# Kernel optimization log

Hardware: AMD Instinct MI355X
Metric: run time of the kernel (lower is better)

Reference implementation:

```python
import jax, jax.numpy as jnp
import numpy as np

B, S, D = 4, 4096, 512
NUM_RANDOM = 32
SEED = 42
SCALE = 1.0 / float(np.sqrt(D))


def _make_random_mask(seq_len, num_random, seed):
    # Faithful to module semantics: diagonal always attended, plus up to
    # (num_random-1) randomly sampled earlier positions per row.
    rng = np.random.default_rng(seed)
    mask = np.zeros((seq_len, seq_len), dtype=bool)
    mask[np.arange(seq_len), np.arange(seq_len)] = True
    for i in range(1, seq_len):
        n = min(num_random - 1, i)
        cols = rng.choice(i, size=n, replace=False)
        mask[i, cols] = True
    return mask


def setup_inputs() -> dict:
    key = jax.random.key(0)
    kq, kk, kv = jax.random.split(key, 3)
    q = jax.random.normal(kq, (B, S, D), dtype=jnp.float32)
    k = jax.random.normal(kk, (B, S, D), dtype=jnp.float32)
    v = jax.random.normal(kv, (B, S, D), dtype=jnp.float32)
    mask = jnp.asarray(_make_random_mask(S, NUM_RANDOM, SEED))  # [S, S] bool
    return {"q": q, "k": k, "v": v, "mask": mask}


def reference(q, k, v, mask):
    # scores: [B, S, S]
    scores = jnp.einsum("bqd,bkd->bqk", q, k) * SCALE
    scores = jnp.where(mask[None, :, :], scores, -jnp.inf)
    attn = jax.nn.softmax(scores, axis=-1)  # every row has >=1 True (diag)
    out = jnp.einsum("bqk,bkd->bqd", attn, v)
    return out, attn, mask
```

## Files before the change

### kernel.cpp

```cpp
#include <hip/hip_runtime.h>
#include <hip/hip_fp16.h>


#define SDIM 4096
#define DDIM 512
#define BATCH 4
#define CCAP 128
#define NREC 32
#define RECSTRIDE 68

#define DT_BF16 0
#define DT_FP16 1
#define DT_FP32 2

#define OUT_ELEMS ((size_t)BATCH * SDIM * DDIM)

__device__ __forceinline__ float bf2f(unsigned int u) {
    return __uint_as_float((u & 0xFFFFu) << 16);
}
__device__ __forceinline__ float h2f(unsigned int u) {
    __half_raw hr; hr.x = (unsigned short)(u & 0xFFFFu);
    return __half2float(hr);
}
__device__ __forceinline__ float decode16(unsigned int bits, int dt) {
    return (dt == DT_BF16) ? bf2f(bits) : h2f(bits);
}

__device__ __forceinline__ bool elem_nz(const unsigned char* m, int w, int i, int j) {
    const unsigned char* p = m + ((size_t)i * SDIM + (size_t)j) * w;
    unsigned v = p[0];
    if (w >= 2) v |= p[1];
    if (w == 4) { v |= p[2]; v |= p[3]; }
    return v != 0;
}
__device__ void detect_mask(const unsigned char* m, int* w_out, int* inv_out) {
    for (int wi = 0; wi < 3; ++wi) {
        const int W = 1 << wi;
        for (int s = 0; s < 2; ++s) {
            const bool att_nz = (s == 0);
            bool ok = true;
            ok &= (elem_nz(m, W, 0, 0) == att_nz);
            ok &= (elem_nz(m, W, 0, 1) != att_nz);
            ok &= (elem_nz(m, W, 0, 2) != att_nz);
            ok &= (elem_nz(m, W, 0, 3) != att_nz);
            ok &= (elem_nz(m, W, 1, 0) == att_nz);
            ok &= (elem_nz(m, W, 1, 1) == att_nz);
            ok &= (elem_nz(m, W, 1, 2) != att_nz);
            ok &= (elem_nz(m, W, 1, 3) != att_nz);
            if (ok) { *w_out = W; *inv_out = s; return; }
        }
    }
    *w_out = 1; *inv_out = 0;
}

#define QG 68

__device__ __forceinline__ void v_accum(
    const unsigned char* __restrict__ vb, int b, int t, int dt,
    const int* __restrict__ cols, const float* __restrict__ probs, int n,
    float& acc0, float& acc1)
{
    acc0 = 0.f; acc1 = 0.f;
    if (dt == DT_FP32) {
        const float2* vbase = (const float2*)((const float*)vb + (size_t)b * SDIM * DDIM);
        int j = 0;
        for (; j + 8 <= n; j += 8) {
            float2 vv[8]; float pp[8];
            #pragma unroll
            for (int u = 0; u < 8; ++u) {
                vv[u] = vbase[(size_t)cols[j + u] * (DDIM / 2) + t];
                pp[u] = probs[j + u];
            }
            #pragma unroll
            for (int u = 0; u < 8; ++u) {
                acc0 += pp[u] * vv[u].x;
                acc1 += pp[u] * vv[u].y;
            }
        }
        for (; j < n; ++j) {
            float2 vv = vbase[(size_t)cols[j] * (DDIM / 2) + t];
            acc0 += probs[j] * vv.x; acc1 += probs[j] * vv.y;
        }
    } else {
        const unsigned short* vb16 = (const unsigned short*)vb;
        int j = 0;
        for (; j + 8 <= n; j += 8) {
            unsigned int vv[8]; float pp[8];
            #pragma unroll
            for (int u = 0; u < 8; ++u) {
                vv[u] = ((const unsigned int*)(vb16 + ((size_t)b * SDIM + cols[j + u]) * DDIM))[t];
                pp[u] = probs[j + u];
            }
            #pragma unroll
            for (int u = 0; u < 8; ++u) {
                acc0 += pp[u] * decode16(vv[u], dt);
                acc1 += pp[u] * decode16(vv[u] >> 16, dt);
            }
        }
        for (; j < n; ++j) {
            unsigned int vv = ((const unsigned int*)(vb16 + ((size_t)b * SDIM + cols[j]) * DDIM))[t];
            acc0 += probs[j] * decode16(vv, dt);
            acc1 += probs[j] * decode16(vv >> 16, dt);
        }
    }
}

__global__ __launch_bounds__(256, 8) void score_kernel(
    const unsigned char* __restrict__ qb,
    const unsigned char* __restrict__ kb,
    const unsigned char* __restrict__ vb,
    const unsigned char* __restrict__ mask,
    float* __restrict__ out,
    float* __restrict__ rec_base,
    long long rec_stride,
    int write_attn)
{
    const int row = blockIdx.x;
    const int b = row >> 12;
    const int i = row & (SDIM - 1);
    const int t = threadIdx.x;
    const int lane = t & 63;
    const int wv = t >> 6;

    __shared__ float q_lds[8 * QG];
    __shared__ int   cols[CCAP];
    __shared__ float scores[CCAP];
    __shared__ float red[4];
    __shared__ int count;
    __shared__ int s_dt;

    if (t == 0) count = 0;
    if (t < 64) {
        unsigned int w = ((const unsigned int*)qb)[t];
        unsigned int by = (w >> 8) & 0x7Fu;
        int cnt_top = __popcll(__ballot(by == 0x3Eu || by == 0x3Fu));
        int cnt_mid = __popcll(__ballot(by >= 0x34u && by <= 0x43u));
        if (t == 0)
            s_dt = (cnt_top >= 20) ? DT_BF16 : ((cnt_mid >= 25) ? DT_FP16 : DT_FP32);
    }
    int mw, minv;
    detect_mask(mask, &mw, &minv);
    __syncthreads();
    const int dt = s_dt;

    if (dt == DT_FP32) {
        float2 qv = ((const float2*)((const float*)qb + ((size_t)b * SDIM + i) * DDIM))[t];
        const int e = 2 * t, a = (e >> 6) * QG + (e & 63);
        q_lds[a] = qv.x; q_lds[a + 1] = qv.y;
    } else {
        unsigned int qv = ((const unsigned int*)((const unsigned short*)qb
                            + ((size_t)b * SDIM + i) * DDIM))[t];
        const int e = 2 * t, a = (e >> 6) * QG + (e & 63);
        q_lds[a] = decode16(qv, dt); q_lds[a + 1] = decode16(qv >> 16, dt);
    }

    if (mw == 1) {
        const unsigned char* mrow = mask + (size_t)i * SDIM;
        uint4 mv = ((const uint4*)mrow)[t];
        unsigned int wd[4] = {mv.x, mv.y, mv.z, mv.w};
        #pragma unroll
        for (int c = 0; c < 4; ++c)
            #pragma unroll
            for (int bi = 0; bi < 4; ++bi) {
                bool nz = ((wd[c] >> (8 * bi)) & 0xFFu) != 0;
                if (nz != (bool)minv) {
                    int pos = atomicAdd(&count, 1);
                    if (pos < CCAP) cols[pos] = t * 16 + c * 4 + bi;
                }
            }
    } else if (mw == 2) {
        const unsigned short* mrow = (const unsigned short*)mask + (size_t)i * SDIM;
        const uint4* m4 = (const uint4*)mrow + t * 2;
        #pragma unroll
        for (int c = 0; c < 2; ++c) {
            uint4 mv = m4[c];
            unsigned int e[4] = {mv.x, mv.y, mv.z, mv.w};
            #pragma unroll
            for (int bi = 0; bi < 4; ++bi) {
                const int base = t * 16 + c * 8 + bi * 2;
                if (((e[bi] & 0xFFFFu) != 0) != (bool)minv) { int p = atomicAdd(&count, 1); if (p < CCAP) cols[p] = base; }
                if (((e[bi] >> 16) != 0)     != (bool)minv) { int p = atomicAdd(&count, 1); if (p < CCAP) cols[p] = base + 1; }
            }
        }
    } else {
        const unsigned int* mrow = (const unsigned int*)mask + (size_t)i * SDIM;
        const uint4* m4 = (const uint4*)mrow + t * 4;
        #pragma unroll
        for (int c = 0; c < 4; ++c) {
            uint4 mv = m4[c];
            unsigned int e[4] = {mv.x, mv.y, mv.z, mv.w};
            #pragma unroll
            for (int bi = 0; bi < 4; ++bi) {
                if ((e[bi] != 0u) != (bool)minv) {
                    int p = atomicAdd(&count, 1);
                    if (p < CCAP) cols[p] = t * 16 + c * 4 + bi;
                }
            }
        }
    }
    __syncthreads();
    const int n = min(count, CCAP);

    const float SCALE = 0.04419417382415922f;
    const int idx = t >> 3, sub = t & 7;
    for (int base = 0; base < n; base += 32) {
        const int j = base + idx;
        float partial = 0.f;
        if (j < n) {
            const size_t koff = ((size_t)b * SDIM + cols[j]) * DDIM;
            if (dt == DT_FP32) {
                const float4* k4 = (const float4*)((const float*)kb + koff) + sub * 16;
                #pragma unroll
                for (int c = 0; c < 16; ++c) {
                    float4 kv = k4[c]; const int dbase = sub * QG + c * 4;
                    partial += kv.x * q_lds[dbase]     + kv.y * q_lds[dbase + 1]
                             + kv.z * q_lds[dbase + 2] + kv.w * q_lds[dbase + 3];
                }
            } else {
                const uint4* k4 = (const uint4*)((const unsigned short*)kb + koff) + sub * 8;
                #pragma unroll
                for (int c = 0; c < 8; ++c) {
                    uint4 kv = k4[c]; const int dbase = sub * QG + c * 8;
                    partial += decode16(kv.x, dt)       * q_lds[dbase]
                             + decode16(kv.x >> 16, dt) * q_lds[dbase + 1]
                             + decode16(kv.y, dt)       * q_lds[dbase + 2]
                             + decode16(kv.y >> 16, dt) * q_lds[dbase + 3]
                             + decode16(kv.z, dt)       * q_lds[dbase + 4]
                             + decode16(kv.z >> 16, dt) * q_lds[dbase + 5]
                             + decode16(kv.w, dt)       * q_lds[dbase + 6]
                             + decode16(kv.w >> 16, dt) * q_lds[dbase + 7];
                }
            }
        }
        partial += __shfl_xor(partial, 1);
        partial += __shfl_xor(partial, 2);
        partial += __shfl_xor(partial, 4);
        if (sub == 0 && j < n) scores[j] = partial * SCALE;
    }
    __syncthreads();

    const float NEG_INF = __int_as_float(0xff800000);
    float lmax = NEG_INF;
    for (int j = t; j < n; j += 256) lmax = fmaxf(lmax, scores[j]);
    #pragma unroll
    for (int off = 1; off < 64; off <<= 1) lmax = fmaxf(lmax, __shfl_xor(lmax, off));
    if (lane == 0) red[wv] = lmax;
    __syncthreads();
    const float M = fmaxf(fmaxf(red[0], red[1]), fmaxf(red[2], red[3]));
    __syncthreads();
    float lsum = 0.f;
    for (int j = t; j < n; j += 256) {
        const float e = __expf(scores[j] - M);
        scores[j] = e;
        lsum += e;
    }
    #pragma unroll
    for (int off = 1; off < 64; off <<= 1) lsum += __shfl_xor(lsum, off);
    if (lane == 0) red[wv] = lsum;
    __syncthreads();
    const float Z = red[0] + red[1] + red[2] + red[3];
    const float invZ = (Z > 0.f) ? 1.f / Z : 0.f;

    if (write_attn) {
        float* arow = rec_base + (size_t)row * rec_stride;
        const int nr = min(n, NREC);
        if (t == 0) arow[0] = __int_as_float(nr);
        if (t < nr) {
            arow[1 + t]  = __int_as_float(cols[t]);
            arow[33 + t] = scores[t] * invZ;
        }
    }

    float acc0, acc1;
    v_accum(vb, b, t, dt, cols, scores, n, acc0, acc1);
    ((float2*)(out + (size_t)row * DDIM))[t] = make_float2(acc0 * invZ, acc1 * invZ);
}

__global__ __launch_bounds__(256) void expand2_kernel(
    const float* __restrict__ rec_base, long long rec_stride,
    float* __restrict__ attn, float* __restrict__ maskout, int do_mask)
{
    const int row = blockIdx.x;
    const int t = threadIdx.x;
    const unsigned int* ar = (const unsigned int*)(rec_base + (size_t)row * rec_stride);

    __shared__ float dense[SDIM];
    __shared__ int   scols[NREC];
    __shared__ float sprob[NREC];
    __shared__ int   sn;

    if (t < NREC) {
        scols[t] = (int)ar[1 + t];
        sprob[t] = __uint_as_float(ar[33 + t]);
    }
    if (t == 64) sn = (int)ar[0];

    float4* d4 = (float4*)dense;
    const float4 z4 = make_float4(0.f, 0.f, 0.f, 0.f);
    #pragma unroll
    for (int r = 0; r < 4; ++r) d4[t + 256 * r] = z4;
    __syncthreads();

    const int n = min(sn, NREC);
    if (t < n) dense[scols[t] & (SDIM - 1)] = sprob[t];
    __syncthreads();

    float4* a4 = (float4*)(attn + (size_t)row * SDIM);
    #pragma unroll
    for (int r = 0; r < 4; ++r) a4[t + 256 * r] = d4[t + 256 * r];

    if (do_mask && (row >> 12) == 0) {
        __syncthreads();
        if (t < n) dense[scols[t] & (SDIM - 1)] = 1.0f;
        __syncthreads();
        float4* m4 = (float4*)(maskout + (size_t)row * SDIM);
        #pragma unroll
        for (int r = 0; r < 4; ++r) m4[t + 256 * r] = d4[t + 256 * r];
    }
}

extern "C" void kernel_launch(void* const* d_in, const int* in_sizes, int n_in,
                              void* d_out, int out_size, void* d_ws, size_t ws_size,
                              hipStream_t stream) {
    const unsigned char* pool[3] = {nullptr, nullptr, nullptr};
    const unsigned char* mask = nullptr;
    int np = 0;
    for (int ii = 0; ii < n_in; ++ii) {
        if (in_sizes[ii] == SDIM * SDIM) mask = (const unsigned char*)d_in[ii];
        else if (np < 3) pool[np++] = (const unsigned char*)d_in[ii];
    }
    if (!mask || np < 3) {
        pool[0] = (const unsigned char*)d_in[0];
        pool[1] = (const unsigned char*)d_in[1];
        pool[2] = (const unsigned char*)d_in[2];
        mask    = (const unsigned char*)d_in[3];
    }
    float* out = (float*)d_out;

    const long long sz_out  = (long long)BATCH * SDIM * DDIM;
    const long long sz_attn = (long long)BATCH * SDIM * SDIM;
    const long long sz_mask = (long long)SDIM * SDIM;
    const int write_attn = (out_size >= (int)(sz_out + sz_attn)) ? 1 : 0;
    const int write_mask = (out_size >= (int)(sz_out + sz_attn + sz_mask)) ? 1 : 0;

    const size_t rec_bytes = (size_t)BATCH * SDIM * RECSTRIDE * sizeof(float);
    float* rec_base;
    long long rec_stride;
    if (d_ws && ws_size >= rec_bytes) {
        rec_base = (float*)d_ws;
        rec_stride = RECSTRIDE;
    } else {
        rec_base = out + sz_out;
        rec_stride = SDIM;
    }

    score_kernel<<<BATCH * SDIM, 256, 0, stream>>>(
        pool[0], pool[1], pool[2], mask, out, rec_base, rec_stride, write_attn);

    if (write_attn)
        expand2_kernel<<<BATCH * SDIM, 256, 0, stream>>>(
            rec_base, rec_stride, out + sz_out, out + sz_out + sz_attn, write_mask);
}
```

Measured before the change: 750.0 us.

## Pre-convert K and V to fp16 in workspace before sparse attention gather

Adds a conversion kernel that rewrites K and V into fp16 copies in the workspace, and the score kernel then gathers these half-width rows for the dot products and the V accumulation. The aim is to halve the bytes fetched per random gather, at the price of one extra full read and write pass over K and V and lower precision for fp32 inputs. The expand kernel also writes the mask output in the same loop as the attention rows instead of after extra barriers and a second scatter.

```diff
diff --git a/kernel.cpp b/kernel.cpp
--- a/kernel.cpp
+++ b/kernel.cpp
@@ -53,15 +53,63 @@
     *w_out = 1; *inv_out = 0;
 }
 
+__device__ __forceinline__ void probe_dtype(const unsigned char* src, int t, int* s_dt) {
+    if (t < 64) {
+        unsigned int w = ((const unsigned int*)src)[t];
+        unsigned int by = (w >> 8) & 0x7Fu;
+        int cnt_top = __popcll(__ballot(by == 0x3Eu || by == 0x3Fu));
+        int cnt_mid = __popcll(__ballot(by >= 0x34u && by <= 0x43u));
+        if (t == 0)
+            *s_dt = (cnt_top >= 20) ? DT_BF16 : ((cnt_mid >= 25) ? DT_FP16 : DT_FP32);
+    }
+}
+
 #define QG 68
 
+__global__ __launch_bounds__(256) void convert_kernel(
+    const unsigned char* __restrict__ kb,
+    const unsigned char* __restrict__ vb,
+    __half* __restrict__ k16,
+    __half* __restrict__ v16)
+{
+    __shared__ int s_dt;
+    const int t = threadIdx.x;
+    probe_dtype(kb, t, &s_dt);
+    __syncthreads();
+    const int dt = s_dt;
+
+    const int blk = blockIdx.x;
+    const unsigned char* src = (blk < 4096) ? kb : vb;
+    __half* dst = (blk < 4096) ? k16 : v16;
+    const size_t base = (size_t)(blk & 4095) * 2048 + (size_t)t * 8;
+
+    __half2* d2 = (__half2*)(dst + base);
+    if (dt == DT_FP32) {
+        const float4* s4 = (const float4*)((const float*)src + base);
+        float4 a = s4[0], b4 = s4[1];
+        d2[0] = __floats2half2_rn(a.x, a.y);
+        d2[1] = __floats2half2_rn(a.z, a.w);
+        d2[2] = __floats2half2_rn(b4.x, b4.y);
+        d2[3] = __floats2half2_rn(b4.z, b4.w);
+    } else if (dt == DT_FP16) {
+        ((uint4*)(dst + base))[0] =
+            ((const uint4*)((const unsigned short*)src + base))[0];
+    } else {
+        uint4 w = ((const uint4*)((const unsigned short*)src + base))[0];
+        unsigned int ww[4] = {w.x, w.y, w.z, w.w};
+        #pragma unroll
+        for (int c = 0; c < 4; ++c)
+            d2[c] = __floats2half2_rn(bf2f(ww[c]), bf2f(ww[c] >> 16));
+    }
+}
+
 __device__ __forceinline__ void v_accum(
-    const unsigned char* __restrict__ vb, int b, int t, int dt,
+    const unsigned char* __restrict__ vb, int b, int t, int dtkv,
     const int* __restrict__ cols, const float* __restrict__ probs, int n,
     float& acc0, float& acc1)
 {
     acc0 = 0.f; acc1 = 0.f;
-    if (dt == DT_FP32) {
+    if (dtkv == DT_FP32) {
         const float2* vbase = (const float2*)((const float*)vb + (size_t)b * SDIM * DDIM);
         int j = 0;
         for (; j + 8 <= n; j += 8) {
@@ -93,14 +141,14 @@
             }
             #pragma unroll
             for (int u = 0; u < 8; ++u) {
-                acc0 += pp[u] * decode16(vv[u], dt);
-                acc1 += pp[u] * decode16(vv[u] >> 16, dt);
+                acc0 += pp[u] * decode16(vv[u], dtkv);
+                acc1 += pp[u] * decode16(vv[u] >> 16, dtkv);
             }
         }
         for (; j < n; ++j) {
             unsigned int vv = ((const unsigned int*)(vb16 + ((size_t)b * SDIM + cols[j]) * DDIM))[t];
-            acc0 += probs[j] * decode16(vv, dt);
-            acc1 += probs[j] * decode16(vv >> 16, dt);
+            acc0 += probs[j] * decode16(vv, dtkv);
+            acc1 += probs[j] * decode16(vv >> 16, dtkv);
         }
     }
 }
@@ -113,7 +161,8 @@
     float* __restrict__ out,
     float* __restrict__ rec_base,
     long long rec_stride,
-    int write_attn)
+    int write_attn,
+    int kv16)
 {
     const int row = blockIdx.x;
     const int b = row >> 12;
@@ -130,18 +179,12 @@
     __shared__ int s_dt;
 
     if (t == 0) count = 0;
-    if (t < 64) {
-        unsigned int w = ((const unsigned int*)qb)[t];
-        unsigned int by = (w >> 8) & 0x7Fu;
-        int cnt_top = __popcll(__ballot(by == 0x3Eu || by == 0x3Fu));
-        int cnt_mid = __popcll(__ballot(by >= 0x34u && by <= 0x43u));
-        if (t == 0)
-            s_dt = (cnt_top >= 20) ? DT_BF16 : ((cnt_mid >= 25) ? DT_FP16 : DT_FP32);
-    }
+    probe_dtype(qb, t, &s_dt);
     int mw, minv;
     detect_mask(mask, &mw, &minv);
     __syncthreads();
     const int dt = s_dt;
+    const int dtkv = kv16 ? DT_FP16 : dt;
 
     if (dt == DT_FP32) {
         float2 qv = ((const float2*)((const float*)qb + ((size_t)b * SDIM + i) * DDIM))[t];
@@ -208,7 +251,7 @@
         float partial = 0.f;
         if (j < n) {
             const size_t koff = ((size_t)b * SDIM + cols[j]) * DDIM;
-            if (dt == DT_FP32) {
+            if (dtkv == DT_FP32) {
                 const float4* k4 = (const float4*)((const float*)kb + koff) + sub * 16;
                 #pragma unroll
                 for (int c = 0; c < 16; ++c) {
@@ -221,14 +264,14 @@
                 #pragma unroll
                 for (int c = 0; c < 8; ++c) {
                     uint4 kv = k4[c]; const int dbase = sub * QG + c * 8;
-                    partial += decode16(kv.x, dt)       * q_lds[dbase]
-                             + decode16(kv.x >> 16, dt) * q_lds[dbase + 1]
-                             + decode16(kv.y, dt)       * q_lds[dbase + 2]
-                             + decode16(kv.y >> 16, dt) * q_lds[dbase + 3]
-                             + decode16(kv.z, dt)       * q_lds[dbase + 4]
-                             + decode16(kv.z >> 16, dt) * q_lds[dbase + 5]
-                             + decode16(kv.w, dt)       * q_lds[dbase + 6]
-                             + decode16(kv.w >> 16, dt) * q_lds[dbase + 7];
+                    partial += decode16(kv.x, dtkv)       * q_lds[dbase]
+                             + decode16(kv.x >> 16, dtkv) * q_lds[dbase + 1]
+                             + decode16(kv.y, dtkv)       * q_lds[dbase + 2]
+                             + decode16(kv.y >> 16, dtkv) * q_lds[dbase + 3]
+                             + decode16(kv.z, dtkv)       * q_lds[dbase + 4]
+                             + decode16(kv.z >> 16, dtkv) * q_lds[dbase + 5]
+                             + decode16(kv.w, dtkv)       * q_lds[dbase + 6]
+                             + decode16(kv.w >> 16, dtkv) * q_lds[dbase + 7];
                 }
             }
         }
@@ -272,7 +315,7 @@
     }
 
     float acc0, acc1;
-    v_accum(vb, b, t, dt, cols, scores, n, acc0, acc1);
+    v_accum(vb, b, t, dtkv, cols, scores, n, acc0, acc1);
     ((float2*)(out + (size_t)row * DDIM))[t] = make_float2(acc0 * invZ, acc1 * invZ);
 }
 
@@ -306,16 +349,17 @@
     __syncthreads();
 
     float4* a4 = (float4*)(attn + (size_t)row * SDIM);
+    const bool domask = do_mask && (row >> 12) == 0;
+    float4* m4 = (float4*)(maskout + (size_t)row * SDIM);
     #pragma unroll
-    for (int r = 0; r < 4; ++r) a4[t + 256 * r] = d4[t + 256 * r];
-
-    if (do_mask && (row >> 12) == 0) {
-        __syncthreads();
-        if (t < n) dense[scols[t] & (SDIM - 1)] = 1.0f;
-        __syncthreads();
-        float4* m4 = (float4*)(maskout + (size_t)row * SDIM);
-        #pragma unroll
-        for (int r = 0; r < 4; ++r) m4[t + 256 * r] = d4[t + 256 * r];
+    for (int r = 0; r < 4; ++r) {
+        float4 dv = d4[t + 256 * r];
+        a4[t + 256 * r] = dv;
+        if (domask)
+            m4[t + 256 * r] = make_float4(dv.x != 0.f ? 1.f : 0.f,
+                                          dv.y != 0.f ? 1.f : 0.f,
+                                          dv.z != 0.f ? 1.f : 0.f,
+                                          dv.w != 0.f ? 1.f : 0.f);
     }
 }
 
@@ -343,10 +387,27 @@
     const int write_attn = (out_size >= (int)(sz_out + sz_attn)) ? 1 : 0;
     const int write_mask = (out_size >= (int)(sz_out + sz_attn + sz_mask)) ? 1 : 0;
 
+    const size_t NE = (size_t)BATCH * SDIM * DDIM;
+    const size_t kv_bytes  = 2 * NE * sizeof(__half);
     const size_t rec_bytes = (size_t)BATCH * SDIM * RECSTRIDE * sizeof(float);
+
+    const unsigned char* kp = pool[1];
+    const unsigned char* vp = pool[2];
+    int kv16 = 0;
     float* rec_base;
     long long rec_stride;
-    if (d_ws && ws_size >= rec_bytes) {
+    unsigned char* wsb = (unsigned char*)d_ws;
+
+    if (d_ws && ws_size >= kv_bytes + rec_bytes) {
+        kv16 = 1;
+        __half* k16 = (__half*)wsb;
+        __half* v16 = (__half*)(wsb + NE * sizeof(__half));
+        convert_kernel<<<8192, 256, 0, stream>>>(pool[1], pool[2], k16, v16);
+        kp = (const unsigned char*)k16;
+        vp = (const unsigned char*)v16;
+        rec_base = (float*)(wsb + kv_bytes);
+        rec_stride = RECSTRIDE;
+    } else if (d_ws && ws_size >= rec_bytes) {
         rec_base = (float*)d_ws;
         rec_stride = RECSTRIDE;
     } else {
@@ -355,7 +416,7 @@
     }
 
     score_kernel<<<BATCH * SDIM, 256, 0, stream>>>(
-        pool[0], pool[1], pool[2], mask, out, rec_base, rec_stride, write_attn);
+        pool[0], kp, vp, mask, out, rec_base, rec_stride, write_attn, kv16);
 
     if (write_attn)
         expand2_kernel<<<BATCH * SDIM, 256, 0, stream>>>(
```

Result: slower. 1.039 ms (+38.6%).

## Fuse dense attention expansion into score kernel and swizzle block-to-row mapping

Applied to the files above, without the earlier changes.

Removes the separate expand kernel and the intermediate sparse record buffer, so the score kernel itself builds the dense attention row in shared memory and writes the attn and mask outputs directly. It also remaps block indices so that consecutive blocks interleave batches and sequence halves. The goal is to drop a kernel launch and the record round-trip through memory. The cost is 16KB of extra LDS per block, which lowers occupancy for the score/V-gather phase, and the memory-bound dense writes now share a kernel with the gather work.

```diff
diff --git a/kernel.cpp b/kernel.cpp
--- a/kernel.cpp
+++ b/kernel.cpp
@@ -6,8 +6,6 @@
 #define DDIM 512
 #define BATCH 4
 #define CCAP 128
-#define NREC 32
-#define RECSTRIDE 68
 
 #define DT_BF16 0
 #define DT_FP16 1
@@ -53,15 +51,26 @@
     *w_out = 1; *inv_out = 0;
 }
 
+__device__ __forceinline__ void probe_dtype(const unsigned char* src, int t, int* s_dt) {
+    if (t < 64) {
+        unsigned int w = ((const unsigned int*)src)[t];
+        unsigned int by = (w >> 8) & 0x7Fu;
+        int cnt_top = __popcll(__ballot(by == 0x3Eu || by == 0x3Fu));
+        int cnt_mid = __popcll(__ballot(by >= 0x34u && by <= 0x43u));
+        if (t == 0)
+            *s_dt = (cnt_top >= 20) ? DT_BF16 : ((cnt_mid >= 25) ? DT_FP16 : DT_FP32);
+    }
+}
+
 #define QG 68
 
 __device__ __forceinline__ void v_accum(
-    const unsigned char* __restrict__ vb, int b, int t, int dt,
+    const unsigned char* __restrict__ vb, int b, int t, int dtkv,
     const int* __restrict__ cols, const float* __restrict__ probs, int n,
     float& acc0, float& acc1)
 {
     acc0 = 0.f; acc1 = 0.f;
-    if (dt == DT_FP32) {
+    if (dtkv == DT_FP32) {
         const float2* vbase = (const float2*)((const float*)vb + (size_t)b * SDIM * DDIM);
         int j = 0;
         for (; j + 8 <= n; j += 8) {
@@ -93,14 +102,14 @@
             }
             #pragma unroll
             for (int u = 0; u < 8; ++u) {
-                acc0 += pp[u] * decode16(vv[u], dt);
-                acc1 += pp[u] * decode16(vv[u] >> 16, dt);
+                acc0 += pp[u] * decode16(vv[u], dtkv);
+                acc1 += pp[u] * decode16(vv[u] >> 16, dtkv);
             }
         }
         for (; j < n; ++j) {
             unsigned int vv = ((const unsigned int*)(vb16 + ((size_t)b * SDIM + cols[j]) * DDIM))[t];
-            acc0 += probs[j] * decode16(vv, dt);
-            acc1 += probs[j] * decode16(vv >> 16, dt);
+            acc0 += probs[j] * decode16(vv, dtkv);
+            acc1 += probs[j] * decode16(vv >> 16, dtkv);
         }
     }
 }
@@ -111,11 +120,11 @@
     const unsigned char* __restrict__ vb,
     const unsigned char* __restrict__ mask,
     float* __restrict__ out,
-    float* __restrict__ rec_base,
-    long long rec_stride,
-    int write_attn)
+    int write_attn,
+    int write_mask)
 {
-    const int row = blockIdx.x;
+    const int g = blockIdx.x;
+    const int row = (((g >> 1) & 3) << 12) | ((g & 1) << 11) | (g >> 3);
     const int b = row >> 12;
     const int i = row & (SDIM - 1);
     const int t = threadIdx.x;
@@ -123,6 +132,7 @@
     const int wv = t >> 6;
 
     __shared__ float q_lds[8 * QG];
+    __shared__ float dense[SDIM];
     __shared__ int   cols[CCAP];
     __shared__ float scores[CCAP];
     __shared__ float red[4];
@@ -130,14 +140,7 @@
     __shared__ int s_dt;
 
     if (t == 0) count = 0;
-    if (t < 64) {
-        unsigned int w = ((const unsigned int*)qb)[t];
-        unsigned int by = (w >> 8) & 0x7Fu;
-        int cnt_top = __popcll(__ballot(by == 0x3Eu || by == 0x3Fu));
-        int cnt_mid = __popcll(__ballot(by >= 0x34u && by <= 0x43u));
-        if (t == 0)
-            s_dt = (cnt_top >= 20) ? DT_BF16 : ((cnt_mid >= 25) ? DT_FP16 : DT_FP32);
-    }
+    probe_dtype(qb, t, &s_dt);
     int mw, minv;
     detect_mask(mask, &mw, &minv);
     __syncthreads();
@@ -262,61 +265,33 @@
     const float invZ = (Z > 0.f) ? 1.f / Z : 0.f;
 
     if (write_attn) {
-        float* arow = rec_base + (size_t)row * rec_stride;
-        const int nr = min(n, NREC);
-        if (t == 0) arow[0] = __int_as_float(nr);
-        if (t < nr) {
-            arow[1 + t]  = __int_as_float(cols[t]);
-            arow[33 + t] = scores[t] * invZ;
+        float4* d4 = (float4*)dense;
+        const float4 z4 = make_float4(0.f, 0.f, 0.f, 0.f);
+        #pragma unroll
+        for (int r = 0; r < 4; ++r) d4[t + 256 * r] = z4;
+        __syncthreads();
+        if (t < n) dense[cols[t] & (SDIM - 1)] = scores[t] * invZ;
+        __syncthreads();
+
+        float4* a4 = (float4*)(out + OUT_ELEMS + (size_t)row * SDIM);
+        const bool domask = write_mask && (b == 0);
+        float4* m4 = (float4*)(out + OUT_ELEMS + (size_t)BATCH * SDIM * SDIM
+                               + (size_t)i * SDIM);
+        #pragma unroll
+        for (int r = 0; r < 4; ++r) {
+            float4 dv = d4[t + 256 * r];
+            a4[t + 256 * r] = dv;
+            if (domask)
+                m4[t + 256 * r] = make_float4(dv.x != 0.f ? 1.f : 0.f,
+                                              dv.y != 0.f ? 1.f : 0.f,
+                                              dv.z != 0.f ? 1.f : 0.f,
+                                              dv.w != 0.f ? 1.f : 0.f);
         }
     }
 
     float acc0, acc1;
     v_accum(vb, b, t, dt, cols, scores, n, acc0, acc1);
     ((float2*)(out + (size_t)row * DDIM))[t] = make_float2(acc0 * invZ, acc1 * invZ);
-}
-
-__global__ __launch_bounds__(256) void expand2_kernel(
-    const float* __restrict__ rec_base, long long rec_stride,
-    float* __restrict__ attn, float* __restrict__ maskout, int do_mask)
-{
-    const int row = blockIdx.x;
-    const int t = threadIdx.x;
-    const unsigned int* ar = (const unsigned int*)(rec_base + (size_t)row * rec_stride);
-
-    __shared__ float dense[SDIM];
-    __shared__ int   scols[NREC];
-    __shared__ float sprob[NREC];
-    __shared__ int   sn;
-
-    if (t < NREC) {
-        scols[t] = (int)ar[1 + t];
-        sprob[t] = __uint_as_float(ar[33 + t]);
-    }
-    if (t == 64) sn = (int)ar[0];
-
-    float4* d4 = (float4*)dense;
-    const float4 z4 = make_float4(0.f, 0.f, 0.f, 0.f);
-    #pragma unroll
-    for (int r = 0; r < 4; ++r) d4[t + 256 * r] = z4;
-    __syncthreads();
-
-    const int n = min(sn, NREC);
-    if (t < n) dense[scols[t] & (SDIM - 1)] = sprob[t];
-    __syncthreads();
-
-    float4* a4 = (float4*)(attn + (size_t)row * SDIM);
-    #pragma unroll
-    for (int r = 0; r < 4; ++r) a4[t + 256 * r] = d4[t + 256 * r];
-
-    if (do_mask && (row >> 12) == 0) {
-        __syncthreads();
-        if (t < n) dense[scols[t] & (SDIM - 1)] = 1.0f;
-        __syncthreads();
-        float4* m4 = (float4*)(maskout + (size_t)row * SDIM);
-        #pragma unroll
-        for (int r = 0; r < 4; ++r) m4[t + 256 * r] = d4[t + 256 * r];
-    }
 }
 
 extern "C" void kernel_launch(void* const* d_in, const int* in_sizes, int n_in,
@@ -343,21 +318,6 @@
     const int write_attn = (out_size >= (int)(sz_out + sz_attn)) ? 1 : 0;
     const int write_mask = (out_size >= (int)(sz_out + sz_attn + sz_mask)) ? 1 : 0;
 
-    const size_t rec_bytes = (size_t)BATCH * SDIM * RECSTRIDE * sizeof(float);
-    float* rec_base;
-    long long rec_stride;
-    if (d_ws && ws_size >= rec_bytes) {
-        rec_base = (float*)d_ws;
-        rec_stride = RECSTRIDE;
-    } else {
-        rec_base = out + sz_out;
-        rec_stride = SDIM;
-    }
-
     score_kernel<<<BATCH * SDIM, 256, 0, stream>>>(
-        pool[0], pool[1], pool[2], mask, out, rec_base, rec_stride, write_attn);
-
-    if (write_attn)
-        expand2_kernel<<<BATCH * SDIM, 256, 0, stream>>>(
-            rec_base, rec_stride, out + sz_out, out + sz_out + sz_attn, write_mask);
-}
+        pool[0], pool[1], pool[2], mask, out, write_attn, write_mask);
+}
```

Result: slower. 771.1 us (+2.8%).
